# Kernel optimization log

Measured on AMD Instinct MI355X. Metric: run time of the kernel, lower is better.

The kernel has to match this reference:

```python
import jax, jax.numpy as jnp
from jax import lax
import numpy as np

B, C, L, K = 4, 4096, 4096, 4
PAD = K - 1  # causal padding = 3


def setup_inputs() -> dict:
    key = jax.random.key(0)
    k1, k2, k3 = jax.random.split(key, 3)
    x = jax.random.normal(k1, (B, C, L), dtype=jnp.float32)
    # HF layout: [kernel_size, 1, channels]; lecun_normal over fan_in = kernel_size
    kernel = jax.random.normal(k2, (K, 1, C), dtype=jnp.float32) / np.sqrt(K)
    bias = jax.random.normal(k3, (C,), dtype=jnp.float32) * 0.02
    return {"x": x, "kernel": kernel, "bias": bias}


def reference(x, kernel, bias):
    # Depthwise causal 1D conv: kernel (K,1,C) -> OIW (C,1,K), groups=C.
    rhs = jnp.swapaxes(kernel, 0, 2)  # (C, 1, K)
    y = lax.conv_general_dilated(
        lhs=x,
        rhs=rhs,
        window_strides=(1,),
        padding=((PAD, PAD),),
        rhs_dilation=(1,),
        feature_group_count=C,
    )  # (B, C, L + 2*PAD - (K-1)) = (B, C, L+3)
    y = y + bias[None, :, None]
    return y.astype(x.dtype)
```

## Files before the change

kernel.cpp:

```cpp
#include <hip/hip_runtime.h>


#define CONV_L 4096
#define CONV_C 4096
#define CONV_OUTL 4099

__global__ __launch_bounds__(256) void conv1d_dw_kernel(
    const float* __restrict__ x,
    const float* __restrict__ kern,
    const float* __restrict__ bias,
    float* __restrict__ out)
{
    const int row = blockIdx.x;
    const int c   = row & (CONV_C - 1);

    const float w0 = kern[c];
    const float w1 = kern[CONV_C + c];
    const float w2 = kern[2 * CONV_C + c];
    const float w3 = kern[3 * CONV_C + c];
    const float bv = bias[c];

    const float* __restrict__ xr = x + (size_t)row * CONV_L;
    float* __restrict__ yr       = out + (size_t)row * CONV_OUTL;

    for (int g = threadIdx.x; g <= 1024; g += 256) {
        const int t0 = g << 2;

        float4 a, b;
        if (t0 >= 4) {
            a = *reinterpret_cast<const float4*>(xr + t0 - 4);
        } else {
            a = make_float4(0.f, 0.f, 0.f, 0.f);
        }
        if (t0 < CONV_L) {
            b = *reinterpret_cast<const float4*>(xr + t0);
        } else {
            b = make_float4(0.f, 0.f, 0.f, 0.f);
        }

        const float y0 = fmaf(w0, a.y, fmaf(w1, a.z, fmaf(w2, a.w, fmaf(w3, b.x, bv))));
        const float y1 = fmaf(w0, a.z, fmaf(w1, a.w, fmaf(w2, b.x, fmaf(w3, b.y, bv))));
        const float y2 = fmaf(w0, a.w, fmaf(w1, b.x, fmaf(w2, b.y, fmaf(w3, b.z, bv))));
        const float y3 = fmaf(w0, b.x, fmaf(w1, b.y, fmaf(w2, b.z, fmaf(w3, b.w, bv))));

        if (t0 + 3 < CONV_OUTL) {
            yr[t0]     = y0;
            yr[t0 + 1] = y1;
            yr[t0 + 2] = y2;
            yr[t0 + 3] = y3;
        } else {
            yr[t0]     = y0;
            yr[t0 + 1] = y1;
            yr[t0 + 2] = y2;
        }
    }
}

extern "C" void kernel_launch(void* const* d_in, const int* in_sizes, int n_in,
                              void* d_out, int out_size, void* d_ws, size_t ws_size,
                              hipStream_t stream)
{
    const float* x    = (const float*)d_in[0];
    const float* kern = (const float*)d_in[1];
    const float* bias = (const float*)d_in[2];
    float* out        = (float*)d_out;

    const int rows = 4 * CONV_C;
    conv1d_dw_kernel<<<rows, 256, 0, stream>>>(x, kern, bias, out);
}
```

Baseline: 102.6 us.

## Align output stores per row phase with vectorized nontemporal float4 writes

Output rows have length 4099, so a row's start address shifts by 3 floats per row and the old scalar stores were misaligned. The kernel now offsets each thread's work by the row's phase (row & 3), so every store is a 16-byte aligned float4 written with a nontemporal hint. Each thread computes 8 outputs from three float4 loads. The up to three leftover edge outputs per row are handled by a small scalar path in the first threads. The input loads then become misaligned in exchange, and the boundary logic grows more complex.

Result: faster. 99.67 us (-2.8%).

```diff
diff --git a/kernel.cpp b/kernel.cpp
--- a/kernel.cpp
+++ b/kernel.cpp
@@ -4,6 +4,16 @@
 #define CONV_L 4096
 #define CONV_C 4096
 #define CONV_OUTL 4099
+
+typedef float f4 __attribute__((ext_vector_type(4)));
+
+__device__ __forceinline__ float xget(const float* __restrict__ xr, int i) {
+    return (i >= 0 && i < CONV_L) ? xr[i] : 0.0f;
+}
+
+__device__ __forceinline__ f4 mkf4(float a, float b, float c, float d) {
+    f4 v; v.x = a; v.y = b; v.z = c; v.w = d; return v;
+}
 
 __global__ __launch_bounds__(256) void conv1d_dw_kernel(
     const float* __restrict__ x,
@@ -13,6 +23,7 @@
 {
     const int row = blockIdx.x;
     const int c   = row & (CONV_C - 1);
+    const int s   = row & 3;
 
     const float w0 = kern[c];
     const float w1 = kern[CONV_C + c];
@@ -23,36 +34,51 @@
     const float* __restrict__ xr = x + (size_t)row * CONV_L;
     float* __restrict__ yr       = out + (size_t)row * CONV_OUTL;
 
-    for (int g = threadIdx.x; g <= 1024; g += 256) {
-        const int t0 = g << 2;
+    if (threadIdx.x < 3) {
+        const int t = (threadIdx.x < (unsigned)s) ? (int)threadIdx.x
+                                                  : (int)(4096 + threadIdx.x);
+        if (t < CONV_OUTL) {
+            float y = bv;
+            y = fmaf(w0, xget(xr, t - 3), y);
+            y = fmaf(w1, xget(xr, t - 2), y);
+            y = fmaf(w2, xget(xr, t - 1), y);
+            y = fmaf(w3, xget(xr, t    ), y);
+            yr[t] = y;
+        }
+    }
 
-        float4 a, b;
-        if (t0 >= 4) {
-            a = *reinterpret_cast<const float4*>(xr + t0 - 4);
+#pragma unroll
+    for (int it = 0; it < 2; ++it) {
+        const int p  = (int)threadIdx.x + it * 256;
+        const int t0 = s + (p << 3);
+
+        f4 a, b, cc;
+        b = *(const f4*)(xr + t0);
+        if (p == 0) {
+            a = mkf4(xget(xr, s - 4), xget(xr, s - 3),
+                     xget(xr, s - 2), xget(xr, s - 1));
         } else {
-            a = make_float4(0.f, 0.f, 0.f, 0.f);
+            a = *(const f4*)(xr + t0 - 4);
         }
-        if (t0 < CONV_L) {
-            b = *reinterpret_cast<const float4*>(xr + t0);
+        if (p == 511 && s != 0) {
+            cc = mkf4(xget(xr, t0 + 4), xget(xr, t0 + 5),
+                      xget(xr, t0 + 6), xget(xr, t0 + 7));
         } else {
-            b = make_float4(0.f, 0.f, 0.f, 0.f);
+            cc = *(const f4*)(xr + t0 + 4);
         }
 
-        const float y0 = fmaf(w0, a.y, fmaf(w1, a.z, fmaf(w2, a.w, fmaf(w3, b.x, bv))));
-        const float y1 = fmaf(w0, a.z, fmaf(w1, a.w, fmaf(w2, b.x, fmaf(w3, b.y, bv))));
-        const float y2 = fmaf(w0, a.w, fmaf(w1, b.x, fmaf(w2, b.y, fmaf(w3, b.z, bv))));
-        const float y3 = fmaf(w0, b.x, fmaf(w1, b.y, fmaf(w2, b.z, fmaf(w3, b.w, bv))));
+        f4 y0, y1;
+        y0.x = fmaf(w0, a.y,  fmaf(w1, a.z,  fmaf(w2, a.w,  fmaf(w3, b.x,  bv))));
+        y0.y = fmaf(w0, a.z,  fmaf(w1, a.w,  fmaf(w2, b.x,  fmaf(w3, b.y,  bv))));
+        y0.z = fmaf(w0, a.w,  fmaf(w1, b.x,  fmaf(w2, b.y,  fmaf(w3, b.z,  bv))));
+        y0.w = fmaf(w0, b.x,  fmaf(w1, b.y,  fmaf(w2, b.z,  fmaf(w3, b.w,  bv))));
+        y1.x = fmaf(w0, b.y,  fmaf(w1, b.z,  fmaf(w2, b.w,  fmaf(w3, cc.x, bv))));
+        y1.y = fmaf(w0, b.z,  fmaf(w1, b.w,  fmaf(w2, cc.x, fmaf(w3, cc.y, bv))));
+        y1.z = fmaf(w0, b.w,  fmaf(w1, cc.x, fmaf(w2, cc.y, fmaf(w3, cc.z, bv))));
+        y1.w = fmaf(w0, cc.x, fmaf(w1, cc.y, fmaf(w2, cc.z, fmaf(w3, cc.w, bv))));
 
-        if (t0 + 3 < CONV_OUTL) {
-            yr[t0]     = y0;
-            yr[t0 + 1] = y1;
-            yr[t0 + 2] = y2;
-            yr[t0 + 3] = y3;
-        } else {
-            yr[t0]     = y0;
-            yr[t0 + 1] = y1;
-            yr[t0 + 2] = y2;
-        }
+        __builtin_nontemporal_store(y0, (f4*)(yr + t0));
+        __builtin_nontemporal_store(y1, (f4*)(yr + t0 + 4));
     }
 }
 
```
